# Optimization experiments

Measured on AMD Instinct MI355X. Metric: run time of the kernel, lower is better.

Reference implementation:

```python
import jax, jax.numpy as jnp
import numpy as np

D0 = 64      # l0 feature channels (state dim)
KC = 3       # l1 (vector) input channels (grads)
EDGE = 32    # edge embedding dim
H, DH = 4, 16
RBF = 16
MAXB = 4
SIG = 0.5
BIG = 1e9
EPS = 1e-5


def _forward(seq, xyz, aamask, num_bonds, state, grads, top_k,
             We, be, Wq, Wk, Wv0, Wv1, Wo0, Wself, b0):
    B, L, A = xyz.shape[:3]
    M = B * L * A
    x = xyz.reshape(M, 3)
    mask = aamask[seq].reshape(M)                                  # [M] bool: which atoms exist
    node0 = state.reshape(M, D0)                                   # l0 features
    l1 = jnp.transpose(grads, (1, 2, 3, 0, 4)).reshape(M, KC, 3)   # l1 (vector) features, [M,KC,3]

    # --- top-k atom graph over masked atoms (dense relaxation of make_atom_graph) ---
    d2 = jnp.sum((x[:, None, :] - x[None, :, :]) ** 2, -1)         # [M,M]
    valid = mask[:, None] & mask[None, :]
    d2m = jnp.where(valid, d2, BIG)
    ii = jnp.arange(M)
    d2m = d2m.at[ii, ii].set(BIG)                                  # exclude self-edges
    neg, idx = jax.lax.top_k(-d2m, top_k)                          # idx: [M,K] nearest masked atoms
    edge_ok = (-neg) < (BIG * 0.5)                                 # [M,K]

    rel = x[idx] - x[:, None, :]                                   # [M,K,3]
    dist = jnp.sqrt(jnp.sum(rel * rel, -1) + EPS)
    dirv = rel / dist[..., None]

    # --- edge features: distance RBF + intra-residue bond-count one-hot ---
    mus = jnp.linspace(0.0, 6.0, RBF)
    rbf = jnp.exp(-((dist[..., None] - mus) ** 2) / (2.0 * SIG * SIG))
    ri = ii // A
    ai = ii % A
    rj = idx // A
    aj = idx % A
    nbr = num_bonds[seq.reshape(-1)]                               # [B*L, A, A]
    bond = jnp.where(rj == ri[:, None], nbr[ri[:, None], ai[:, None], aj], 0)
    e = jnp.concatenate([rbf, jax.nn.one_hot(jnp.clip(bond, 0, MAXB), MAXB + 1)], -1)
    e = e @ We + be                                                # [M,K,EDGE]

    # --- SE(3)-invariant scalars from l1 features ---
    l1j = l1[idx]                                                  # [M,K,KC,3]
    inv = jnp.einsum('mkcd,mkd->mkc', l1j, dirv)                   # [M,K,KC]
    norms = jnp.sqrt(jnp.sum(l1 * l1, -1) + EPS)                   # [M,KC]

    # --- equivariant multi-head attention over neighbors ---
    kin = jnp.concatenate([node0[idx], e, inv], -1)                # [M,K,D0+EDGE+KC]
    qin = jnp.concatenate([node0, norms], -1)                      # [M,D0+KC]
    q = (qin @ Wq).reshape(M, H, DH)
    k = (kin @ Wk).reshape(M, top_k, H, DH)
    v0 = (kin @ Wv0).reshape(M, top_k, H, DH)
    v1 = (kin @ Wv1).reshape(M, top_k, H, 1 + KC)

    logits = jnp.einsum('mhd,mkhd->mhk', q, k) / float(np.sqrt(DH))
    logits = jnp.where(edge_ok[:, None, :], logits, -1e9)
    attn = jax.nn.softmax(logits, -1)                              # [M,H,K]

    o0 = jnp.einsum('mhk,mkhd->mhd', attn, v0).reshape(M, H * DH)
    out0 = o0 @ Wo0 + node0 @ Wself + b0                           # new l0 / state  [M,D0]

    coef = jnp.einsum('mhk,mkhc->mkc', attn, v1)                   # invariant coefs [M,K,1+KC]
    vmsg = coef[..., :1] * dirv + jnp.einsum('mkc,mkcd->mkd', coef[..., 1:], l1j)
    out1 = jnp.sum(vmsg, 1)                                        # l1 output shift [M,3]

    # --- scatter back through the mask (state[mask] = ...; xyz[mask] += shift/100) ---
    state_new = jnp.where(mask[:, None], out0, node0).reshape(B, L, A, D0)
    xyz_new = jnp.where(mask[:, None], x + out1 / 100.0, x).reshape(B, L, A, 3)
    return xyz_new, state_new


def setup_inputs() -> dict:
    key = jax.random.key(0)
    ks = jax.random.split(key, 16)
    B, L, A, NAA = 1, 256, 36, 21
    seq = jax.random.randint(ks[0], (B, L), 0, NAA)
    xyz = jax.random.normal(ks[1], (B, L, A, 3), jnp.float32)
    aamask = jax.random.uniform(ks[2], (NAA, A)) < 0.45
    num_bonds = jax.random.randint(ks[3], (NAA, A, A), 0, MAXB + 1)
    state = jax.random.normal(ks[4], (B, L, A, D0), jnp.float32)
    grads = jax.random.normal(ks[5], (KC, B, L, A, 3), jnp.float32)
    s = 0.05
    KIN = D0 + EDGE + KC
    QIN = D0 + KC
    We = s * jax.random.normal(ks[6], (RBF + MAXB + 1, EDGE), jnp.float32)
    be = jnp.zeros((EDGE,), jnp.float32)
    Wq = s * jax.random.normal(ks[7], (QIN, H * DH), jnp.float32)
    Wk = s * jax.random.normal(ks[8], (KIN, H * DH), jnp.float32)
    Wv0 = s * jax.random.normal(ks[9], (KIN, H * DH), jnp.float32)
    Wv1 = s * jax.random.normal(ks[10], (KIN, H * (1 + KC)), jnp.float32)
    Wo0 = s * jax.random.normal(ks[11], (H * DH, D0), jnp.float32)
    Wself = s * jax.random.normal(ks[12], (D0, D0), jnp.float32)
    b0 = jnp.zeros((D0,), jnp.float32)
    return {"seq": seq, "xyz": xyz, "aamask": aamask, "num_bonds": num_bonds,
            "state": state, "grads": grads, "top_k": 24,
            "We": We, "be": be, "Wq": Wq, "Wk": Wk, "Wv0": Wv0, "Wv1": Wv1,
            "Wo0": Wo0, "Wself": Wself, "b0": b0}


def reference(seq, xyz, aamask, num_bonds, state, grads, top_k,
              We, be, Wq, Wk, Wv0, Wv1, Wo0, Wself, b0):
    return _forward(seq, xyz, aamask, num_bonds, state, grads, top_k,
                    We, be, Wq, Wk, Wv0, Wv1, Wo0, Wself, b0)
```

## Files before the change

kernel.cpp:

```cpp
#include <hip/hip_runtime.h>
#include <math.h>

#define MTOT 9216
#define A_ 36
#define D0_ 64
#define EDGE_ 32
#define RBF_ 16
#define KNN 24
#define QIN_ 67
#define EPS_ 1e-5f

__global__ void k_zero(int* cnt) { if (threadIdx.x == 0) *cnt = 0; }

__global__ void k_prep(const int* __restrict__ seq, const float* __restrict__ xyz,
                       const int* __restrict__ aamask,
                       float4* __restrict__ pact, float* __restrict__ out_xyz,
                       int* __restrict__ cnt) {
    int m = blockIdx.x * blockDim.x + threadIdx.x;
    if (m >= MTOT) return;
    int r = m / A_;
    int a = m - r * A_;
    int mk = (aamask[seq[r] * A_ + a] != 0);
    float x0 = xyz[m * 3 + 0], x1 = xyz[m * 3 + 1], x2 = xyz[m * 3 + 2];
    out_xyz[m * 3 + 0] = x0;
    out_xyz[m * 3 + 1] = x1;
    out_xyz[m * 3 + 2] = x2;
    if (mk) {
        int p = atomicAdd(cnt, 1);
        pact[p] = make_float4(x0, x1, x2, __int_as_float(m));
    }
}

__global__ void k_copy(const float4* __restrict__ src, float4* __restrict__ dst, int n4) {
    int t = blockIdx.x * blockDim.x + threadIdx.x;
    if (t < n4) dst[t] = src[t];
}

#define CAP 128
#define WPB 4

__global__ __launch_bounds__(256) void k_nbr(const float4* __restrict__ pact,
                                             const int* __restrict__ cnt,
                                             int* __restrict__ idx) {
    __shared__ uint2 s_cand[WPB][CAP];

    const int nact = *cnt;
    const int lane = threadIdx.x & 63;
    const int wv = threadIdx.x >> 6;
    const int slot = blockIdx.x * WPB + wv;
    if (slot >= nact) return;

    const float4 pq = pact[slot];
    const int ia = __float_as_int(pq.w);
    const unsigned long long lmask = (1ULL << lane) - 1ULL;

    unsigned cum[32];
    #pragma unroll
    for (int b = 0; b < 32; ++b) cum[b] = 0u;

    for (int base = 0; base < nact; base += 64) {
        int c = base + lane;
        float4 p = pact[c];
        int j = __float_as_int(p.w);
        float dx = p.x - pq.x, dy = p.y - pq.y, dz = p.z - pq.z;
        float d2 = dx * dx + dy * dy + dz * dz;
        unsigned bits = __float_as_uint(d2);
        int bb = min(max((int)(bits >> 22) - 240, 0), 31);
        unsigned bin = (c < nact && j != ia) ? (unsigned)bb : 1000u;
        #pragma unroll
        for (int b = 0; b < 32; ++b)
            cum[b] += (unsigned)__popcll(__ballot(bin <= (unsigned)b));
    }

    int bstar = 31;
    #pragma unroll
    for (int b = 31; b >= 0; --b) if (cum[b] >= KNN) bstar = b;
    const unsigned limit = (unsigned)(241 + bstar) << 22;

    int nsel = 0;
    for (int base = 0; base < nact; base += 64) {
        int c = base + lane;
        float4 p = pact[c];
        int j = __float_as_int(p.w);
        float dx = p.x - pq.x, dy = p.y - pq.y, dz = p.z - pq.z;
        float d2 = dx * dx + dy * dy + dz * dz;
        unsigned bits = __float_as_uint(d2);
        bool sel = (c < nact) && (j != ia) && (bits < limit);
        unsigned long long m = __ballot(sel);
        int pos = nsel + (int)__popcll(m & lmask);
        if (sel && pos < CAP) s_cand[wv][pos] = make_uint2(bits, (unsigned)j);
        nsel += (int)__popcll(m);
    }
    __builtin_amdgcn_wave_barrier();

    int n = min(nsel, CAP);
    for (int c = lane; c < n; c += 64) {
        uint2 my = s_cand[wv][c];
        int rank = 0;
        for (int c2 = 0; c2 < n; ++c2) {
            uint2 o = s_cand[wv][c2];
            rank += (o.x < my.x) || (o.x == my.x && o.y < my.y);
        }
        if (rank < KNN) idx[ia * KNN + rank] = (int)my.y;
    }
}

__global__ __launch_bounds__(64, 2) void k_attn(
    const float* __restrict__ xyz, const int* __restrict__ seq,
    const int* __restrict__ num_bonds, const float* __restrict__ state,
    const float* __restrict__ grads,
    const float* __restrict__ We, const float* __restrict__ be,
    const float* __restrict__ Wq, const float* __restrict__ Wk,
    const float* __restrict__ Wv0, const float* __restrict__ Wv1,
    const float* __restrict__ Wo0, const float* __restrict__ Wself,
    const float* __restrict__ b0,
    const float4* __restrict__ pact, const int* __restrict__ cnt,
    const int* __restrict__ idxbuf,
    float* __restrict__ out_xyz, float* __restrict__ out_state) {
    const int nact = *cnt;
    if ((int)blockIdx.x >= nact) return;
    const int i = __float_as_int(pact[blockIdx.x].w);
    const int lane = threadIdx.x;
    const int l15 = lane & 15;
    const int h = lane >> 4;

    __shared__ float s_kin[KNN][100];
    __shared__ float s_qw[4][100];
    __shared__ float s_wkin[4][100];
    __shared__ float s_dir[KNN][4];
    __shared__ float s_rbf[KNN][RBF_];
    __shared__ float s_l1j[KNN][3][3];
    __shared__ float s_qin[68];
    __shared__ float s_q[64];
    __shared__ float s_logit[4][KNN];
    __shared__ float s_attn[4][KNN];
    __shared__ float s_o0[64];
    __shared__ float s_v1[KNN][16];
    __shared__ float s_coef[KNN][4];
    __shared__ int   s_j[KNN];
    __shared__ int   s_ok[KNN];
    __shared__ int   s_bc[KNN];
    __shared__ float s_xi[3];

    s_qin[lane] = state[i * D0_ + lane];
    if (lane < 3) {
        float g0 = grads[(lane * MTOT + i) * 3 + 0];
        float g1 = grads[(lane * MTOT + i) * 3 + 1];
        float g2 = grads[(lane * MTOT + i) * 3 + 2];
        s_qin[D0_ + lane] = sqrtf(g0 * g0 + g1 * g1 + g2 * g2 + EPS_);
        s_xi[lane] = xyz[i * 3 + lane];
    }
    if (lane < KNN) {
        int j = idxbuf[i * KNN + lane];
        int ok = (j >= 0 && j < MTOT);
        int jj = ok ? j : 0;
        s_j[lane] = jj;
        s_ok[lane] = ok;
        float dx = xyz[jj * 3 + 0] - xyz[i * 3 + 0];
        float dy = xyz[jj * 3 + 1] - xyz[i * 3 + 1];
        float dz = xyz[jj * 3 + 2] - xyz[i * 3 + 2];
        float dist = sqrtf(dx * dx + dy * dy + dz * dz + EPS_);
        s_dir[lane][0] = dx / dist;
        s_dir[lane][1] = dy / dist;
        s_dir[lane][2] = dz / dist;
        s_dir[lane][3] = dist;
        int ri = i / A_, ai = i - ri * A_;
        int rj = jj / A_, aj = jj - rj * A_;
        int b = 0;
        if (rj == ri) b = num_bonds[(seq[ri] * A_ + ai) * A_ + aj];
        s_bc[lane] = min(max(b, 0), 4);
    }
    __syncthreads();

    {
        float q = 0.0f;
        for (int c = 0; c < QIN_; ++c) q += s_qin[c] * Wq[c * 64 + lane];
        s_q[lane] = q;
    }
    for (int f = lane; f < KNN * RBF_; f += 64) {
        int k = f >> 4, r = f & 15;
        float mu = (6.0f / 15.0f) * (float)r;
        float d = s_dir[k][3] - mu;
        s_rbf[k][r] = expf(-d * d * 2.0f);
    }
    for (int k = 0; k < KNN; ++k) s_kin[k][lane] = state[s_j[k] * D0_ + lane];
    for (int f = lane; f < KNN * 3; f += 64) {
        int k = f / 3, c = f - 3 * k;
        int jj = s_j[k];
        float g0 = grads[(c * MTOT + jj) * 3 + 0];
        float g1 = grads[(c * MTOT + jj) * 3 + 1];
        float g2 = grads[(c * MTOT + jj) * 3 + 2];
        s_l1j[k][c][0] = g0; s_l1j[k][c][1] = g1; s_l1j[k][c][2] = g2;
        s_kin[k][96 + c] = g0 * s_dir[k][0] + g1 * s_dir[k][1] + g2 * s_dir[k][2];
    }
    if (lane < KNN) s_kin[lane][99] = 0.0f;
    __syncthreads();

    for (int f = lane; f < KNN * EDGE_; f += 64) {
        int k = f >> 5, d = f & 31;
        float acc = be[d] + We[(RBF_ + s_bc[k]) * EDGE_ + d];
        #pragma unroll
        for (int r = 0; r < RBF_; ++r) acc += s_rbf[k][r] * We[r * EDGE_ + d];
        s_kin[k][64 + d] = acc;
    }
    for (int t = 0; t < 7; ++t) {
        int c = t * 16 + l15;
        if (c < 99) {
            const float* wk = &Wk[c * 64 + h * 16];
            float acc = 0.0f;
            #pragma unroll
            for (int d = 0; d < 16; ++d) acc += s_q[h * 16 + d] * wk[d];
            s_qw[h][c] = acc;
        }
    }
    __syncthreads();

    for (int f = lane; f < 96; f += 64) {
        int k = f >> 2, hh = f & 3;
        const float4* k4 = (const float4*)s_kin[k];
        const float4* q4 = (const float4*)s_qw[hh];
        float acc = 0.0f;
        #pragma unroll
        for (int c4 = 0; c4 < 24; ++c4) {
            float4 a = k4[c4], b = q4[c4];
            acc += a.x * b.x + a.y * b.y + a.z * b.z + a.w * b.w;
        }
        acc += s_kin[k][96] * s_qw[hh][96] + s_kin[k][97] * s_qw[hh][97]
             + s_kin[k][98] * s_qw[hh][98];
        s_logit[hh][k] = s_ok[k] ? acc * 0.25f : -1e9f;
    }
    __syncthreads();

    float attn[KNN];
    {
        float mx = -1e30f;
        #pragma unroll
        for (int k = 0; k < KNN; ++k) { attn[k] = s_logit[h][k]; mx = fmaxf(mx, attn[k]); }
        float ss = 0.0f;
        #pragma unroll
        for (int k = 0; k < KNN; ++k) { attn[k] = expf(attn[k] - mx); ss += attn[k]; }
        float rs = 1.0f / ss;
        #pragma unroll
        for (int k = 0; k < KNN; ++k) attn[k] *= rs;
    }
    s_attn[h][l15] = attn[l15];
    if (l15 < 8) s_attn[h][16 + l15] = attn[16 + l15];

    for (int t = 0; t < 7; ++t) {
        int c = t * 16 + l15;
        if (c < 99) {
            float acc = 0.0f;
            #pragma unroll
            for (int k = 0; k < KNN; ++k) acc += attn[k] * s_kin[k][c];
            s_wkin[h][c] = acc;
        }
    }
    for (int t = 0; t < 6; ++t) {
        int k = (t * 64 + lane) >> 4;
        const float4* k4 = (const float4*)s_kin[k];
        const float* wv = &Wv1[l15];
        float acc = 0.0f;
        #pragma unroll
        for (int c4 = 0; c4 < 24; ++c4) {
            float4 a = k4[c4];
            acc += a.x * wv[(c4 * 4 + 0) * 16] + a.y * wv[(c4 * 4 + 1) * 16]
                 + a.z * wv[(c4 * 4 + 2) * 16] + a.w * wv[(c4 * 4 + 3) * 16];
        }
        acc += s_kin[k][96] * wv[96 * 16] + s_kin[k][97] * wv[97 * 16]
             + s_kin[k][98] * wv[98 * 16];
        s_v1[k][l15] = acc;
    }
    __syncthreads();

    {
        float o0 = 0.0f;
        for (int c = 0; c < 99; ++c) o0 += s_wkin[h][c] * Wv0[c * 64 + lane];
        s_o0[lane] = o0;
    }
    __syncthreads();

    {
        float acc = b0[lane];
        for (int t = 0; t < 64; ++t) acc += s_o0[t] * Wo0[t * 64 + lane];
        for (int t = 0; t < 64; ++t) acc += s_qin[t] * Wself[t * 64 + lane];
        out_state[i * D0_ + lane] = acc;
    }
    for (int f = lane; f < KNN * 4; f += 64) {
        int k = f >> 2, c = f & 3;
        float a2 = 0.0f;
        #pragma unroll
        for (int hh = 0; hh < 4; ++hh) a2 += s_attn[hh][k] * s_v1[k][hh * 4 + c];
        s_coef[k][c] = a2;
    }
    __syncthreads();

    if (lane < 3) {
        float o1 = 0.0f;
        #pragma unroll
        for (int k = 0; k < KNN; ++k) {
            float t = s_coef[k][0] * s_dir[k][lane];
            t += s_coef[k][1] * s_l1j[k][0][lane];
            t += s_coef[k][2] * s_l1j[k][1][lane];
            t += s_coef[k][3] * s_l1j[k][2][lane];
            o1 += t;
        }
        out_xyz[i * 3 + lane] = s_xi[lane] + o1 / 100.0f;
    }
}

extern "C" void kernel_launch(void* const* d_in, const int* in_sizes, int n_in,
                              void* d_out, int out_size, void* d_ws, size_t ws_size,
                              hipStream_t stream) {
    const int*   seq    = (const int*)d_in[0];
    const float* xyz    = (const float*)d_in[1];
    const int*   aamask = (const int*)d_in[2];
    const int*   nbonds = (const int*)d_in[3];
    const float* state  = (const float*)d_in[4];
    const float* grads  = (const float*)d_in[5];
    const float* We    = (const float*)d_in[7];
    const float* be    = (const float*)d_in[8];
    const float* Wq    = (const float*)d_in[9];
    const float* Wk    = (const float*)d_in[10];
    const float* Wv0   = (const float*)d_in[11];
    const float* Wv1   = (const float*)d_in[12];
    const float* Wo0   = (const float*)d_in[13];
    const float* Wself = (const float*)d_in[14];
    const float* b0    = (const float*)d_in[15];

    float* out_xyz   = (float*)d_out;
    float* out_state = out_xyz + MTOT * 3;

    char* ws = (char*)d_ws;
    int*    cnt  = (int*)ws;
    float4* pact = (float4*)(ws + 16);
    int*    idx  = (int*)(ws + 16 + 148480);

    k_zero<<<1, 64, 0, stream>>>(cnt);
    k_prep<<<(MTOT + 255) / 256, 256, 0, stream>>>(seq, xyz, aamask, pact,
                                                   out_xyz, cnt);
    k_copy<<<(MTOT * D0_ / 4 + 255) / 256, 256, 0, stream>>>(
        (const float4*)state, (float4*)out_state, MTOT * D0_ / 4);
    k_nbr<<<(MTOT + WPB - 1) / WPB, 256, 0, stream>>>(pact, cnt, idx);
    k_attn<<<MTOT, 64, 0, stream>>>(xyz, seq, nbonds, state, grads, We, be, Wq, Wk,
                                    Wv0, Wv1, Wo0, Wself, b0, pact, cnt, idx,
                                    out_xyz, out_state);
}
```

Before: 228.7 us.

## Fuse neighbor search into attention kernel and merge state copy into prep

The top-k neighbor search now runs inside the per-atom attention kernel, so selected neighbor indices stay in shared memory instead of passing through a global index buffer. The state copy is folded into the prep kernel, cutting the launch count from five to three. The histogram now uses 16 coarser bins instead of 32, which lowers ballot work and register pressure but can admit more candidates near the threshold. Shared buffers are aliased to shrink LDS use, and the launch_bounds occupancy hint is dropped, which may change per-block scheduling.

```diff
diff --git a/kernel.cpp b/kernel.cpp
--- a/kernel.cpp
+++ b/kernel.cpp
@@ -9,54 +9,73 @@
 #define KNN 24
 #define QIN_ 67
 #define EPS_ 1e-5f
+#define CAP 128
 
 __global__ void k_zero(int* cnt) { if (threadIdx.x == 0) *cnt = 0; }
 
 __global__ void k_prep(const int* __restrict__ seq, const float* __restrict__ xyz,
                        const int* __restrict__ aamask,
+                       const float4* __restrict__ state4, float4* __restrict__ out_state4,
                        float4* __restrict__ pact, float* __restrict__ out_xyz,
                        int* __restrict__ cnt) {
-    int m = blockIdx.x * blockDim.x + threadIdx.x;
-    if (m >= MTOT) return;
-    int r = m / A_;
-    int a = m - r * A_;
-    int mk = (aamask[seq[r] * A_ + a] != 0);
-    float x0 = xyz[m * 3 + 0], x1 = xyz[m * 3 + 1], x2 = xyz[m * 3 + 2];
-    out_xyz[m * 3 + 0] = x0;
-    out_xyz[m * 3 + 1] = x1;
-    out_xyz[m * 3 + 2] = x2;
-    if (mk) {
-        int p = atomicAdd(cnt, 1);
-        pact[p] = make_float4(x0, x1, x2, __int_as_float(m));
+    int t = blockIdx.x * blockDim.x + threadIdx.x;
+    if (t < MTOT * D0_ / 4) out_state4[t] = state4[t];
+    if (t < MTOT) {
+        int r = t / A_;
+        int a = t - r * A_;
+        int mk = (aamask[seq[r] * A_ + a] != 0);
+        float x0 = xyz[t * 3 + 0], x1 = xyz[t * 3 + 1], x2 = xyz[t * 3 + 2];
+        out_xyz[t * 3 + 0] = x0;
+        out_xyz[t * 3 + 1] = x1;
+        out_xyz[t * 3 + 2] = x2;
+        if (mk) {
+            int p = atomicAdd(cnt, 1);
+            pact[p] = make_float4(x0, x1, x2, __int_as_float(t));
+        }
     }
 }
 
-__global__ void k_copy(const float4* __restrict__ src, float4* __restrict__ dst, int n4) {
-    int t = blockIdx.x * blockDim.x + threadIdx.x;
-    if (t < n4) dst[t] = src[t];
-}
-
-#define CAP 128
-#define WPB 4
-
-__global__ __launch_bounds__(256) void k_nbr(const float4* __restrict__ pact,
-                                             const int* __restrict__ cnt,
-                                             int* __restrict__ idx) {
-    __shared__ uint2 s_cand[WPB][CAP];
+__global__ __launch_bounds__(64) void k_main(
+    const float4* __restrict__ pact, const int* __restrict__ cnt,
+    const float* __restrict__ xyz, const int* __restrict__ seq,
+    const int* __restrict__ num_bonds, const float* __restrict__ state,
+    const float* __restrict__ grads,
+    const float* __restrict__ We, const float* __restrict__ be,
+    const float* __restrict__ Wq, const float* __restrict__ Wk,
+    const float* __restrict__ Wv0, const float* __restrict__ Wv1,
+    const float* __restrict__ Wo0, const float* __restrict__ Wself,
+    const float* __restrict__ b0,
+    float* __restrict__ out_xyz, float* __restrict__ out_state) {
 
     const int nact = *cnt;
-    const int lane = threadIdx.x & 63;
-    const int wv = threadIdx.x >> 6;
-    const int slot = blockIdx.x * WPB + wv;
-    if (slot >= nact) return;
-
-    const float4 pq = pact[slot];
+    if ((int)blockIdx.x >= nact) return;
+    const int lane = threadIdx.x;
+    const int l15 = lane & 15;
+    const int h = lane >> 4;
+
+    __shared__ float s_kin[KNN][100];
+    __shared__ float s_u[400];
+    __shared__ float s_wkin[4][100];
+    __shared__ float s_dir[KNN][4];
+    __shared__ float s_l1j[KNN][3][3];
+    __shared__ float s_qin[68];
+    __shared__ float s_qo[64];
+    __shared__ float s_logit[4][KNN];
+    __shared__ float s_attn[4][KNN];
+    __shared__ float s_coef[KNN][4];
+    __shared__ int   s_selj[KNN];
+    __shared__ int   s_bc[KNN];
+    __shared__ float s_xi[3];
+
+    uint2* s_cand = (uint2*)&s_kin[0][0];
+
+    const float4 pq = pact[blockIdx.x];
     const int ia = __float_as_int(pq.w);
     const unsigned long long lmask = (1ULL << lane) - 1ULL;
 
-    unsigned cum[32];
+    unsigned cum[16];
     #pragma unroll
-    for (int b = 0; b < 32; ++b) cum[b] = 0u;
+    for (int b = 0; b < 16; ++b) cum[b] = 0u;
 
     for (int base = 0; base < nact; base += 64) {
         int c = base + lane;
@@ -64,18 +83,16 @@
         int j = __float_as_int(p.w);
         float dx = p.x - pq.x, dy = p.y - pq.y, dz = p.z - pq.z;
         float d2 = dx * dx + dy * dy + dz * dz;
-        unsigned bits = __float_as_uint(d2);
-        int bb = min(max((int)(bits >> 22) - 240, 0), 31);
+        int bb = min(max((int)(__float_as_uint(d2) >> 22) - 240, 0), 31);
         unsigned bin = (c < nact && j != ia) ? (unsigned)bb : 1000u;
         #pragma unroll
-        for (int b = 0; b < 32; ++b)
-            cum[b] += (unsigned)__popcll(__ballot(bin <= (unsigned)b));
-    }
-
-    int bstar = 31;
+        for (int b = 0; b < 16; ++b)
+            cum[b] += (unsigned)__popcll(__ballot(bin <= (unsigned)(2 * b + 1)));
+    }
+    int bsel = 15;
     #pragma unroll
-    for (int b = 31; b >= 0; --b) if (cum[b] >= KNN) bstar = b;
-    const unsigned limit = (unsigned)(241 + bstar) << 22;
+    for (int b = 15; b >= 0; --b) if (cum[b] >= KNN) bsel = b;
+    const unsigned limit = (unsigned)(241 + 2 * bsel + 1) << 22;
 
     int nsel = 0;
     for (int base = 0; base < nact; base += 64) {
@@ -88,59 +105,24 @@
         bool sel = (c < nact) && (j != ia) && (bits < limit);
         unsigned long long m = __ballot(sel);
         int pos = nsel + (int)__popcll(m & lmask);
-        if (sel && pos < CAP) s_cand[wv][pos] = make_uint2(bits, (unsigned)j);
+        if (sel && pos < CAP) s_cand[pos] = make_uint2(bits, (unsigned)j);
         nsel += (int)__popcll(m);
     }
-    __builtin_amdgcn_wave_barrier();
+    __syncthreads();
 
     int n = min(nsel, CAP);
     for (int c = lane; c < n; c += 64) {
-        uint2 my = s_cand[wv][c];
+        uint2 my = s_cand[c];
         int rank = 0;
         for (int c2 = 0; c2 < n; ++c2) {
-            uint2 o = s_cand[wv][c2];
+            uint2 o = s_cand[c2];
             rank += (o.x < my.x) || (o.x == my.x && o.y < my.y);
         }
-        if (rank < KNN) idx[ia * KNN + rank] = (int)my.y;
-    }
-}
-
-__global__ __launch_bounds__(64, 2) void k_attn(
-    const float* __restrict__ xyz, const int* __restrict__ seq,
-    const int* __restrict__ num_bonds, const float* __restrict__ state,
-    const float* __restrict__ grads,
-    const float* __restrict__ We, const float* __restrict__ be,
-    const float* __restrict__ Wq, const float* __restrict__ Wk,
-    const float* __restrict__ Wv0, const float* __restrict__ Wv1,
-    const float* __restrict__ Wo0, const float* __restrict__ Wself,
-    const float* __restrict__ b0,
-    const float4* __restrict__ pact, const int* __restrict__ cnt,
-    const int* __restrict__ idxbuf,
-    float* __restrict__ out_xyz, float* __restrict__ out_state) {
-    const int nact = *cnt;
-    if ((int)blockIdx.x >= nact) return;
-    const int i = __float_as_int(pact[blockIdx.x].w);
-    const int lane = threadIdx.x;
-    const int l15 = lane & 15;
-    const int h = lane >> 4;
-
-    __shared__ float s_kin[KNN][100];
-    __shared__ float s_qw[4][100];
-    __shared__ float s_wkin[4][100];
-    __shared__ float s_dir[KNN][4];
-    __shared__ float s_rbf[KNN][RBF_];
-    __shared__ float s_l1j[KNN][3][3];
-    __shared__ float s_qin[68];
-    __shared__ float s_q[64];
-    __shared__ float s_logit[4][KNN];
-    __shared__ float s_attn[4][KNN];
-    __shared__ float s_o0[64];
-    __shared__ float s_v1[KNN][16];
-    __shared__ float s_coef[KNN][4];
-    __shared__ int   s_j[KNN];
-    __shared__ int   s_ok[KNN];
-    __shared__ int   s_bc[KNN];
-    __shared__ float s_xi[3];
+        if (rank < KNN) s_selj[rank] = (int)my.y;
+    }
+    __syncthreads();
+
+    const int i = ia;
 
     s_qin[lane] = state[i * D0_ + lane];
     if (lane < 3) {
@@ -151,11 +133,7 @@
         s_xi[lane] = xyz[i * 3 + lane];
     }
     if (lane < KNN) {
-        int j = idxbuf[i * KNN + lane];
-        int ok = (j >= 0 && j < MTOT);
-        int jj = ok ? j : 0;
-        s_j[lane] = jj;
-        s_ok[lane] = ok;
+        int jj = s_selj[lane];
         float dx = xyz[jj * 3 + 0] - xyz[i * 3 + 0];
         float dy = xyz[jj * 3 + 1] - xyz[i * 3 + 1];
         float dz = xyz[jj * 3 + 2] - xyz[i * 3 + 2];
@@ -175,18 +153,18 @@
     {
         float q = 0.0f;
         for (int c = 0; c < QIN_; ++c) q += s_qin[c] * Wq[c * 64 + lane];
-        s_q[lane] = q;
+        s_qo[lane] = q;
     }
     for (int f = lane; f < KNN * RBF_; f += 64) {
         int k = f >> 4, r = f & 15;
         float mu = (6.0f / 15.0f) * (float)r;
         float d = s_dir[k][3] - mu;
-        s_rbf[k][r] = expf(-d * d * 2.0f);
-    }
-    for (int k = 0; k < KNN; ++k) s_kin[k][lane] = state[s_j[k] * D0_ + lane];
+        s_u[k * 16 + r] = expf(-d * d * 2.0f);
+    }
+    for (int k = 0; k < KNN; ++k) s_kin[k][lane] = state[s_selj[k] * D0_ + lane];
     for (int f = lane; f < KNN * 3; f += 64) {
         int k = f / 3, c = f - 3 * k;
-        int jj = s_j[k];
+        int jj = s_selj[k];
         float g0 = grads[(c * MTOT + jj) * 3 + 0];
         float g1 = grads[(c * MTOT + jj) * 3 + 1];
         float g2 = grads[(c * MTOT + jj) * 3 + 2];
@@ -200,17 +178,19 @@
         int k = f >> 5, d = f & 31;
         float acc = be[d] + We[(RBF_ + s_bc[k]) * EDGE_ + d];
         #pragma unroll
-        for (int r = 0; r < RBF_; ++r) acc += s_rbf[k][r] * We[r * EDGE_ + d];
+        for (int r = 0; r < RBF_; ++r) acc += s_u[k * 16 + r] * We[r * EDGE_ + d];
         s_kin[k][64 + d] = acc;
     }
+    __syncthreads();
+
     for (int t = 0; t < 7; ++t) {
         int c = t * 16 + l15;
         if (c < 99) {
             const float* wk = &Wk[c * 64 + h * 16];
             float acc = 0.0f;
             #pragma unroll
-            for (int d = 0; d < 16; ++d) acc += s_q[h * 16 + d] * wk[d];
-            s_qw[h][c] = acc;
+            for (int d = 0; d < 16; ++d) acc += s_qo[h * 16 + d] * wk[d];
+            s_u[h * 100 + c] = acc;
         }
     }
     __syncthreads();
@@ -218,16 +198,16 @@
     for (int f = lane; f < 96; f += 64) {
         int k = f >> 2, hh = f & 3;
         const float4* k4 = (const float4*)s_kin[k];
-        const float4* q4 = (const float4*)s_qw[hh];
+        const float4* q4 = (const float4*)&s_u[hh * 100];
         float acc = 0.0f;
         #pragma unroll
         for (int c4 = 0; c4 < 24; ++c4) {
             float4 a = k4[c4], b = q4[c4];
             acc += a.x * b.x + a.y * b.y + a.z * b.z + a.w * b.w;
         }
-        acc += s_kin[k][96] * s_qw[hh][96] + s_kin[k][97] * s_qw[hh][97]
-             + s_kin[k][98] * s_qw[hh][98];
-        s_logit[hh][k] = s_ok[k] ? acc * 0.25f : -1e9f;
+        acc += s_kin[k][96] * s_u[hh * 100 + 96] + s_kin[k][97] * s_u[hh * 100 + 97]
+             + s_kin[k][98] * s_u[hh * 100 + 98];
+        s_logit[hh][k] = acc * 0.25f;
     }
     __syncthreads();
 
@@ -268,20 +248,21 @@
         }
         acc += s_kin[k][96] * wv[96 * 16] + s_kin[k][97] * wv[97 * 16]
              + s_kin[k][98] * wv[98 * 16];
-        s_v1[k][l15] = acc;
+        s_u[k * 16 + l15] = acc;
     }
     __syncthreads();
 
     {
         float o0 = 0.0f;
         for (int c = 0; c < 99; ++c) o0 += s_wkin[h][c] * Wv0[c * 64 + lane];
-        s_o0[lane] = o0;
+        __syncthreads();
+        s_qo[lane] = o0;
     }
     __syncthreads();
 
     {
         float acc = b0[lane];
-        for (int t = 0; t < 64; ++t) acc += s_o0[t] * Wo0[t * 64 + lane];
+        for (int t = 0; t < 64; ++t) acc += s_qo[t] * Wo0[t * 64 + lane];
         for (int t = 0; t < 64; ++t) acc += s_qin[t] * Wself[t * 64 + lane];
         out_state[i * D0_ + lane] = acc;
     }
@@ -289,7 +270,7 @@
         int k = f >> 2, c = f & 3;
         float a2 = 0.0f;
         #pragma unroll
-        for (int hh = 0; hh < 4; ++hh) a2 += s_attn[hh][k] * s_v1[k][hh * 4 + c];
+        for (int hh = 0; hh < 4; ++hh) a2 += s_attn[hh][k] * s_u[k * 16 + hh * 4 + c];
         s_coef[k][c] = a2;
     }
     __syncthreads();
@@ -333,15 +314,12 @@
     char* ws = (char*)d_ws;
     int*    cnt  = (int*)ws;
     float4* pact = (float4*)(ws + 16);
-    int*    idx  = (int*)(ws + 16 + 148480);
 
     k_zero<<<1, 64, 0, stream>>>(cnt);
-    k_prep<<<(MTOT + 255) / 256, 256, 0, stream>>>(seq, xyz, aamask, pact,
-                                                   out_xyz, cnt);
-    k_copy<<<(MTOT * D0_ / 4 + 255) / 256, 256, 0, stream>>>(
-        (const float4*)state, (float4*)out_state, MTOT * D0_ / 4);
-    k_nbr<<<(MTOT + WPB - 1) / WPB, 256, 0, stream>>>(pact, cnt, idx);
-    k_attn<<<MTOT, 64, 0, stream>>>(xyz, seq, nbonds, state, grads, We, be, Wq, Wk,
-                                    Wv0, Wv1, Wo0, Wself, b0, pact, cnt, idx,
+    k_prep<<<(MTOT * D0_ / 4 + 255) / 256, 256, 0, stream>>>(
+        seq, xyz, aamask, (const float4*)state, (float4*)out_state,
+        pact, out_xyz, cnt);
+    k_main<<<MTOT, 64, 0, stream>>>(pact, cnt, xyz, seq, nbonds, state, grads,
+                                    We, be, Wq, Wk, Wv0, Wv1, Wo0, Wself, b0,
                                     out_xyz, out_state);
 }
```

New measurement: 329.1 us. +43.9%, slower.

## Fuse state copy into prep kernel, halve histogram bins in kNN search

Applied to the files above, without the earlier changes.

The zero and copy kernels are dropped: the counter is cleared with a memset and the state copy is folded into the prep kernel, which cuts two launches. In the neighbor kernel the distance histogram now uses 16 coarse bins of two exponent steps each instead of 32, halving the ballot/popcount work per candidate chunk. To make room for the larger candidate sets the coarser threshold admits, the per-wave candidate buffer doubles to 256 entries. The cost is more shared memory per block and a larger quadratic rank sort over the candidates.

```diff
diff --git a/kernel.cpp b/kernel.cpp
--- a/kernel.cpp
+++ b/kernel.cpp
@@ -10,39 +10,35 @@
 #define QIN_ 67
 #define EPS_ 1e-5f
 
-__global__ void k_zero(int* cnt) { if (threadIdx.x == 0) *cnt = 0; }
-
 __global__ void k_prep(const int* __restrict__ seq, const float* __restrict__ xyz,
                        const int* __restrict__ aamask,
+                       const float4* __restrict__ state4, float4* __restrict__ out_state4,
                        float4* __restrict__ pact, float* __restrict__ out_xyz,
                        int* __restrict__ cnt) {
-    int m = blockIdx.x * blockDim.x + threadIdx.x;
-    if (m >= MTOT) return;
-    int r = m / A_;
-    int a = m - r * A_;
-    int mk = (aamask[seq[r] * A_ + a] != 0);
-    float x0 = xyz[m * 3 + 0], x1 = xyz[m * 3 + 1], x2 = xyz[m * 3 + 2];
-    out_xyz[m * 3 + 0] = x0;
-    out_xyz[m * 3 + 1] = x1;
-    out_xyz[m * 3 + 2] = x2;
-    if (mk) {
-        int p = atomicAdd(cnt, 1);
-        pact[p] = make_float4(x0, x1, x2, __int_as_float(m));
+    int t = blockIdx.x * blockDim.x + threadIdx.x;
+    if (t < MTOT * D0_ / 4) out_state4[t] = state4[t];
+    if (t < MTOT) {
+        int r = t / A_;
+        int a = t - r * A_;
+        int mk = (aamask[seq[r] * A_ + a] != 0);
+        float x0 = xyz[t * 3 + 0], x1 = xyz[t * 3 + 1], x2 = xyz[t * 3 + 2];
+        out_xyz[t * 3 + 0] = x0;
+        out_xyz[t * 3 + 1] = x1;
+        out_xyz[t * 3 + 2] = x2;
+        if (mk) {
+            int p = atomicAdd(cnt, 1);
+            pact[p] = make_float4(x0, x1, x2, __int_as_float(t));
+        }
     }
 }
 
-__global__ void k_copy(const float4* __restrict__ src, float4* __restrict__ dst, int n4) {
-    int t = blockIdx.x * blockDim.x + threadIdx.x;
-    if (t < n4) dst[t] = src[t];
-}
-
-#define CAP 128
+#define CAPN 256
 #define WPB 4
 
 __global__ __launch_bounds__(256) void k_nbr(const float4* __restrict__ pact,
                                              const int* __restrict__ cnt,
                                              int* __restrict__ idx) {
-    __shared__ uint2 s_cand[WPB][CAP];
+    __shared__ uint2 s_cand[WPB][CAPN];
 
     const int nact = *cnt;
     const int lane = threadIdx.x & 63;
@@ -54,9 +50,9 @@
     const int ia = __float_as_int(pq.w);
     const unsigned long long lmask = (1ULL << lane) - 1ULL;
 
-    unsigned cum[32];
+    unsigned cum[16];
     #pragma unroll
-    for (int b = 0; b < 32; ++b) cum[b] = 0u;
+    for (int b = 0; b < 16; ++b) cum[b] = 0u;
 
     for (int base = 0; base < nact; base += 64) {
         int c = base + lane;
@@ -64,18 +60,17 @@
         int j = __float_as_int(p.w);
         float dx = p.x - pq.x, dy = p.y - pq.y, dz = p.z - pq.z;
         float d2 = dx * dx + dy * dy + dz * dz;
-        unsigned bits = __float_as_uint(d2);
-        int bb = min(max((int)(bits >> 22) - 240, 0), 31);
+        int bb = min(max((int)(__float_as_uint(d2) >> 22) - 240, 0), 31);
         unsigned bin = (c < nact && j != ia) ? (unsigned)bb : 1000u;
         #pragma unroll
-        for (int b = 0; b < 32; ++b)
-            cum[b] += (unsigned)__popcll(__ballot(bin <= (unsigned)b));
-    }
-
-    int bstar = 31;
+        for (int b = 0; b < 16; ++b)
+            cum[b] += (unsigned)__popcll(__ballot(bin <= (unsigned)(2 * b + 1)));
+    }
+
+    int bsel = 15;
     #pragma unroll
-    for (int b = 31; b >= 0; --b) if (cum[b] >= KNN) bstar = b;
-    const unsigned limit = (unsigned)(241 + bstar) << 22;
+    for (int b = 15; b >= 0; --b) if (cum[b] >= KNN) bsel = b;
+    const unsigned limit = (unsigned)(242 + 2 * bsel) << 22;
 
     int nsel = 0;
     for (int base = 0; base < nact; base += 64) {
@@ -88,12 +83,12 @@
         bool sel = (c < nact) && (j != ia) && (bits < limit);
         unsigned long long m = __ballot(sel);
         int pos = nsel + (int)__popcll(m & lmask);
-        if (sel && pos < CAP) s_cand[wv][pos] = make_uint2(bits, (unsigned)j);
+        if (sel && pos < CAPN) s_cand[wv][pos] = make_uint2(bits, (unsigned)j);
         nsel += (int)__popcll(m);
     }
     __builtin_amdgcn_wave_barrier();
 
-    int n = min(nsel, CAP);
+    int n = min(nsel, CAPN);
     for (int c = lane; c < n; c += 64) {
         uint2 my = s_cand[wv][c];
         int rank = 0;
@@ -333,13 +328,12 @@
     char* ws = (char*)d_ws;
     int*    cnt  = (int*)ws;
     float4* pact = (float4*)(ws + 16);
-    int*    idx  = (int*)(ws + 16 + 148480);
-
-    k_zero<<<1, 64, 0, stream>>>(cnt);
-    k_prep<<<(MTOT + 255) / 256, 256, 0, stream>>>(seq, xyz, aamask, pact,
-                                                   out_xyz, cnt);
-    k_copy<<<(MTOT * D0_ / 4 + 255) / 256, 256, 0, stream>>>(
-        (const float4*)state, (float4*)out_state, MTOT * D0_ / 4);
+    int*    idx  = (int*)(ws + 16 + 149504);
+
+    hipMemsetAsync(cnt, 0, 16, stream);
+    k_prep<<<(MTOT * D0_ / 4 + 255) / 256, 256, 0, stream>>>(
+        seq, xyz, aamask, (const float4*)state, (float4*)out_state,
+        pact, out_xyz, cnt);
     k_nbr<<<(MTOT + WPB - 1) / WPB, 256, 0, stream>>>(pact, cnt, idx);
     k_attn<<<MTOT, 64, 0, stream>>>(xyz, seq, nbonds, state, grads, We, be, Wq, Wk,
                                     Wv0, Wv1, Wo0, Wself, b0, pact, cnt, idx,
```

New measurement: 225.4 us. Within noise of the previous version (-1.4%).
